# Kernel tuning notes

Hardware: AMD Instinct MI355X
Metric: run time of the kernel (lower is better)

The kernel has to match this reference:

```python
import jax, jax.numpy as jnp
import numpy as np
from jax import lax

NL = 32            # number of ocean layers
NFORCING = 720     # hourly forcing steps (30 days)
DT_FORCING = 3600.0
DT = 60.0
NSUB = 60          # dt_forcing // dt
FC_VAL = 1e-4      # Coriolis frequency [s^-1]


def setup_inputs() -> dict:
    key = jax.random.key(0)
    k1, k2, k3 = jax.random.split(key, 3)
    # pk = log(K); keep K in a physically sane range via offset
    pk = jax.random.normal(k1, (2 * NL,), dtype=jnp.float32) * 0.5 - 10.0
    TAx = jax.random.normal(k2, (NFORCING,), dtype=jnp.float32) * 0.1  # wind stress [N/m^2]
    TAy = jax.random.normal(k3, (NFORCING,), dtype=jnp.float32) * 0.1
    fc = jnp.full((1,), FC_VAL, dtype=jnp.float32)
    return {"pk": pk, "TAx": TAx, "TAy": TAy, "fc": fc}


def _vector_field(t, U, V, f, K, TAx, TAy):
    # temporal interpolation of forcing (matches original index arithmetic)
    it = jnp.asarray(t // DT, jnp.int32)
    itf = it // NSUB
    aa = (jnp.mod(it, NSUB) / NSUB).astype(U.dtype)
    nT = TAx.shape[0]
    itsup = jnp.where(itf + 1 >= nT, -1, itf + 1)
    TAxnow = (1 - aa) * TAx[itf] + aa * TAx[itsup]
    TAynow = (1 - aa) * TAy[itf] + aa * TAy[itsup]
    # N-layer stencil (nl > 1 branch of lax.cond), fully vectorized:
    #   layer 0   : +Kin[0]*TA       - Kout[0]*(x0 - x1)
    #   layer k   : -Kin[k]*(xk-xk-1) - Kout[k]*(xk - xk+1)
    #   layer nl-1: -Kin[-1]*(x - x_prev) - Kout[-1]*x   (i.e. x_next = 0)
    Kin, Kout = K[0::2], K[1::2]                       # [nl] each
    zero = jnp.zeros((1,), U.dtype)
    Unext = jnp.concatenate([U[1:], zero])
    Vnext = jnp.concatenate([V[1:], zero])
    dU_top = jnp.concatenate([Kin[:1] * TAxnow, -Kin[1:] * (U[1:] - U[:-1])])
    dV_top = jnp.concatenate([Kin[:1] * TAynow, -Kin[1:] * (V[1:] - V[:-1])])
    d_U = f * V + dU_top - Kout * (U - Unext)
    d_V = -f * U + dV_top - Kout * (V - Vnext)
    return d_U, d_V


def reference(pk, TAx, TAy, fc):
    nl = pk.shape[0] // 2
    K = jnp.exp(pk)
    f = fc[0]
    Nforcing = TAx.shape[0]
    U0 = jnp.zeros((Nforcing, nl), dtype=pk.dtype)
    V0 = jnp.zeros((Nforcing, nl), dtype=pk.dtype)

    def inner(carry, iin):
        Uold, Vold, iout = carry
        t = iout * DT_FORCING + iin * DT
        d_U, d_V = _vector_field(t, Uold, Vold, f, K, TAx, TAy)
        return (Uold + DT * d_U, Vold + DT * d_V, iout), None

    def outer(carry, iout):
        U, V = carry
        (u, v, _), _ = lax.scan(inner, (U[iout], V[iout], iout),
                                jnp.arange(NSUB))
        # last write (iout+1 == Nforcing) is out-of-bounds -> dropped,
        # exactly as in the original .at[].set semantics
        U = U.at[iout + 1].set(u)
        V = V.at[iout + 1].set(v)
        return (U, V), None

    (U, V), _ = lax.scan(outer, (U0, V0), jnp.arange(Nforcing))
    return U, V
```

## Files before the change

kernel.cpp:

```cpp
#include <hip/hip_runtime.h>
#include <hip/hip_bf16.h>

#define NLAYERS 32
#define NFORC   720
#define NSUB    60
#define DTS     60.0f
#define T_CH    16
#define N_CH    45
#define MAGIC   0x1234ABCD
#define SD      34


__device__ __forceinline__ bool sniff_bf16(const void* pk_raw, int lane) {
    const __hip_bfloat16* pk_bf = (const __hip_bfloat16*)pk_raw;
    const float v = __bfloat162float(pk_bf[lane]);
    return __all(v > -30.0f && v < -1.0f);
}

__device__ __forceinline__ void load_mrow(const float2* sMat, int i, int h, float2* R) {
    const float4* rp = (const float4*)(sMat + i * SD + h * 16);
    #pragma unroll
    for (int jj = 0; jj < 8; ++jj) {
        const float4 v = rp[jj];
        R[2 * jj]     = make_float2(v.x, v.y);
        R[2 * jj + 1] = make_float2(v.z, v.w);
    }
}

__device__ __forceinline__ float2 rmatvec(const float2* R, float2 x, int hbase) {
    float a0 = 0.f, a1 = 0.f, a2 = 0.f, a3 = 0.f;
    #pragma unroll
    for (int jj = 0; jj < 16; ++jj) {
        const float xr = __shfl(x.x, hbase + jj);
        const float xi = __shfl(x.y, hbase + jj);
        const float2 m = R[jj];
        a0 = fmaf(m.x, xr, a0);
        a1 = fmaf(m.y, xi, a1);
        a2 = fmaf(m.x, xi, a2);
        a3 = fmaf(m.y, xr, a3);
    }
    float yr = a0 - a1, yi = a2 + a3;
    yr += __shfl_xor(yr, 32);
    yi += __shfl_xor(yi, 32);
    return make_float2(yr, yi);
}

__device__ __forceinline__ void cmatmul8(float2* D, const float2* A, const float2* B, int tt) {
    if ((unsigned)tt < 128u) {
        const int i = tt >> 2, j0 = (tt & 3) * 8;
        float ar[8], ai[8];
        #pragma unroll
        for (int m = 0; m < 8; ++m) { ar[m] = 0.f; ai[m] = 0.f; }
        #pragma unroll 4
        for (int k = 0; k < 32; ++k) {
            const float2 a = A[i * SD + k];
            const float4* bp = (const float4*)(B + k * SD + j0);
            #pragma unroll
            for (int m = 0; m < 4; ++m) {
                const float4 b = bp[m];
                ar[2*m]   = fmaf(a.x, b.x, fmaf(-a.y, b.y, ar[2*m]));
                ai[2*m]   = fmaf(a.x, b.y, fmaf( a.y, b.x, ai[2*m]));
                ar[2*m+1] = fmaf(a.x, b.z, fmaf(-a.y, b.w, ar[2*m+1]));
                ai[2*m+1] = fmaf(a.x, b.w, fmaf( a.y, b.z, ai[2*m+1]));
            }
        }
        float4* dp = (float4*)(D + i * SD + j0);
        #pragma unroll
        for (int m = 0; m < 4; ++m)
            dp[m] = make_float4(ar[2*m], ai[2*m], ar[2*m+1], ai[2*m+1]);
    }
}

__global__ __launch_bounds__(1024, 1)
void junsteak_one(const void* pk_raw, const void* tax_raw, const void* tay_raw,
                  const void* fc_raw, float2* ws_z, int* ws_flag, void* out_raw)
{
    __shared__ __align__(16) float2 sM [NLAYERS * SD];
    __shared__ __align__(16) float2 sB1[NLAYERS * SD];
    __shared__ __align__(16) float2 sB2[NLAYERS * SD];
    __shared__ __align__(16) float2 sCX[NFORC];
    __shared__ __align__(16) float2 sZL[(N_CH - 1) * NLAYERS];
    __shared__ __align__(16) float4 sPQ[NLAYERS];

    const int t = threadIdx.x, lane = t & 63, wv = t >> 6;
    const int l = lane & 31, h = lane >> 5, col = 2 * wv + h;
    const int c = blockIdx.x;
    const int hbase = 16 * h;

    const bool bf = sniff_bf16(pk_raw, lane);

    float kin, kout, f, dtkin0;
    if (bf) {
        const __hip_bfloat16* pk = (const __hip_bfloat16*)pk_raw;
        kin    = expf(__bfloat162float(pk[2 * l]));
        kout   = expf(__bfloat162float(pk[2 * l + 1]));
        f      = __bfloat162float(((const __hip_bfloat16*)fc_raw)[0]);
        dtkin0 = DTS * expf(__bfloat162float(pk[0]));
        const __hip_bfloat16* tx = (const __hip_bfloat16*)tax_raw;
        const __hip_bfloat16* ty = (const __hip_bfloat16*)tay_raw;
        if (t < NFORC)
            sCX[t] = make_float2(__bfloat162float(tx[t]), __bfloat162float(ty[t]));
    } else {
        const float* pk = (const float*)pk_raw;
        kin    = expf(pk[2 * l]);
        kout   = expf(pk[2 * l + 1]);
        f      = ((const float*)fc_raw)[0];
        dtkin0 = DTS * expf(pk[0]);
        const float* tx = (const float*)tax_raw;
        const float* ty = (const float*)tay_raw;
        if (t < NFORC) sCX[t] = make_float2(tx[t], ty[t]);
    }

    __hip_bfloat16* out_bf = (__hip_bfloat16*)out_raw;
    float*          out_f  = (float*)out_raw;
    const int VOFF = NFORC * NLAYERS;

    if (c == 0 && t < 64) {
        const int off = (t >= 32 ? VOFF : 0) + (t & 31);
        if (bf) out_bf[off] = __float2bfloat16(0.0f); else out_f[off] = 0.0f;
    }

    {
        float xr = (l == col) ? 1.0f : 0.0f, xi = 0.0f;
        float Pr = 0.f, Pi = 0.f, Qr = 0.f, Qi = 0.f;
        const bool row0 = (l == 0), row31 = (l == 31);
        for (int m = 0; m < NSUB; ++m) {
            const float cp = dtkin0 * (float)(m + 1) * (1.0f / 60.0f);
            const float cq = dtkin0 * (float)(NSUB - 1 - m) * (1.0f / 60.0f);
            Pr = fmaf(cp, xr, Pr); Pi = fmaf(cp, xi, Pi);
            Qr = fmaf(cq, xr, Qr); Qi = fmaf(cq, xi, Qi);
            float xrm = __shfl_up(xr, 1);
            float xim = __shfl_up(xi, 1);
            float xrp = __shfl_down(xr, 1);
            float xip = __shfl_down(xi, 1);
            if (row31) { xrp = 0.0f; xip = 0.0f; }
            const float Lr = row0 ? (-kout * (xr - xrp))
                                  : (-kin * (xr - xrm) - kout * (xr - xrp));
            const float Li = row0 ? (-kout * (xi - xip))
                                  : (-kin * (xi - xim) - kout * (xi - xip));
            const float nxr = xr + DTS * Lr + DTS * f * xi;
            const float nxi = xi + DTS * Li - DTS * f * xr;
            xr = nxr; xi = nxi;
        }
        sM[l * SD + col] = make_float2(xr, xi);
        if (wv == 0 && h == 0) sPQ[l] = make_float4(Pr, Pi, Qr, Qi);
    }
    __syncthreads();

    float4 pq = make_float4(0.f, 0.f, 0.f, 0.f);
    float2 Mreg[16];
    float2 x = make_float2(0.0f, 0.0f);
    const int a    = c * T_CH;
    const int bend = min(a + T_CH, NFORC - 1);

    if (wv == 0) {
        pq = sPQ[l];
        load_mrow(sM, l, h, Mreg);
        float2 cn = sCX[a];
        for (int s = a; s < bend; ++s) {
            const float2 cs = cn;
            cn = sCX[s + 1];
            const float2 y = rmatvec(Mreg, x, hbase);
            const float gr = pq.x * cs.x - pq.y * cs.y + pq.z * cn.x - pq.w * cn.y;
            const float gi = pq.x * cs.y + pq.y * cs.x + pq.z * cn.y + pq.w * cn.x;
            x = make_float2(y.x + gr, y.y + gi);
        }
        if (h == 0) {
            unsigned long long zu;
            __builtin_memcpy(&zu, &x, 8);
            __hip_atomic_store((unsigned long long*)(ws_z + c * NLAYERS + l), zu,
                               __ATOMIC_RELAXED, __HIP_MEMORY_SCOPE_AGENT);
        }
        __threadfence();
        if (lane == 0)
            __hip_atomic_store(ws_flag + c, (int)MAGIC,
                               __ATOMIC_RELEASE, __HIP_MEMORY_SCOPE_AGENT);
    } else {
        cmatmul8(sB1, sM, sM, t - 64);
    }
    __syncthreads();

    if (wv == 0) {
        if (c > 0) {
            int v;
            do {
                v = (lane < c) ? __hip_atomic_load(ws_flag + lane, __ATOMIC_ACQUIRE,
                                                   __HIP_MEMORY_SCOPE_AGENT)
                               : (int)MAGIC;
            } while (!__all(v == (int)MAGIC));
            for (int idx = lane; idx < c * NLAYERS; idx += 64) {
                const unsigned long long zu =
                    __hip_atomic_load((const unsigned long long*)(ws_z + idx),
                                      __ATOMIC_RELAXED, __HIP_MEMORY_SCOPE_AGENT);
                float2 z;
                __builtin_memcpy(&z, &zu, 8);
                sZL[idx] = z;
            }
        }
    } else {
        cmatmul8(sB2, sB1, sB1, t - 64);
    }
    __syncthreads();

    if (wv != 0) cmatmul8(sB1, sB2, sB2, t - 64);
    __syncthreads();
    if (wv != 0) cmatmul8(sB2, sB1, sB1, t - 64);
    __syncthreads();

    if (t >= 64) return;

    {
        float2 Ereg[16];
        load_mrow(sB2, l, h, Ereg);
        x = make_float2(0.0f, 0.0f);
        for (int j = 0; j < c; ++j) {
            const float2 z = sZL[j * NLAYERS + l];
            const float2 y = rmatvec(Ereg, x, hbase);
            x = make_float2(y.x + z.x, y.y + z.y);
        }
    }

    {
        float2 cn = sCX[a];
        for (int s = a; s < bend; ++s) {
            const float2 cs = cn;
            cn = sCX[s + 1];
            const float2 y = rmatvec(Mreg, x, hbase);
            const float gr = pq.x * cs.x - pq.y * cs.y + pq.z * cn.x - pq.w * cn.y;
            const float gi = pq.x * cs.y + pq.y * cs.x + pq.z * cn.y + pq.w * cn.x;
            x = make_float2(y.x + gr, y.y + gi);
            if (h == 0) {
                const int row = (s + 1) * NLAYERS + l;
                if (bf) {
                    out_bf[row]        = __float2bfloat16(x.x);
                    out_bf[VOFF + row] = __float2bfloat16(x.y);
                } else {
                    out_f[row]        = x.x;
                    out_f[VOFF + row] = x.y;
                }
            }
        }
    }
}

extern "C" void kernel_launch(void* const* d_in, const int* in_sizes, int n_in,
                              void* d_out, int out_size, void* d_ws, size_t ws_size,
                              hipStream_t stream) {
    (void)in_sizes; (void)n_in; (void)out_size; (void)ws_size;
    float2* ws_z   = (float2*)d_ws;
    int*    ws_flg = (int*)((char*)d_ws + (size_t)N_CH * NLAYERS * sizeof(float2));
    junsteak_one<<<dim3(N_CH), dim3(1024), 0, stream>>>(
        d_in[0], d_in[1], d_in[2], d_in[3], ws_z, ws_flg, d_out);
}
```

Measured before the change: 112.7 us.

## Diagonalize layer operator via tridiagonal eigensolve to replace complex matrix powers

Replaces the dense 32x32 complex step-matrix construction and repeated squaring with an eigendecomposition. The symmetrized tridiagonal diffusion operator is solved by multisection bisection plus inverse iteration, so the chunk recurrence becomes scalar complex multiplies per eigenmode. Outputs are mapped back with a real 32x32 eigenvector matvec spread across waves. Chunks grow to 32 steps on 23 blocks of 512 threads, and intra-block handoff uses LDS flags in place of barriers. This assumes the Coriolis term commutes with the diffusion operator and that float32 eigenvectors are accurate enough, which risks numerical error for clustered eigenvalues.

```diff
diff --git a/kernel.cpp b/kernel.cpp
--- a/kernel.cpp
+++ b/kernel.cpp
@@ -4,170 +4,252 @@
 #define NLAYERS 32
 #define NFORC   720
 #define NSUB    60
-#define DTS     60.0f
-#define T_CH    16
-#define N_CH    45
+#define T_CH    32
+#define N_CH    23
 #define MAGIC   0x1234ABCD
-#define SD      34
-
-
+#define GSTR    36
+
+
+__device__ __forceinline__ float rl(float v, int i) {
+    return __int_as_float(__builtin_amdgcn_readlane(__float_as_int(v), i));
+}
+__device__ __forceinline__ float guardf(float x) {
+    const float ax = fabsf(x);
+    return (ax < 1e-28f) ? ((x < 0.f) ? -1e-28f : 1e-28f) : x;
+}
 __device__ __forceinline__ bool sniff_bf16(const void* pk_raw, int lane) {
     const __hip_bfloat16* pk_bf = (const __hip_bfloat16*)pk_raw;
     const float v = __bfloat162float(pk_bf[lane]);
     return __all(v > -30.0f && v < -1.0f);
 }
-
-__device__ __forceinline__ void load_mrow(const float2* sMat, int i, int h, float2* R) {
-    const float4* rp = (const float4*)(sMat + i * SD + h * 16);
-    #pragma unroll
-    for (int jj = 0; jj < 8; ++jj) {
-        const float4 v = rp[jj];
-        R[2 * jj]     = make_float2(v.x, v.y);
-        R[2 * jj + 1] = make_float2(v.z, v.w);
-    }
-}
-
-__device__ __forceinline__ float2 rmatvec(const float2* R, float2 x, int hbase) {
-    float a0 = 0.f, a1 = 0.f, a2 = 0.f, a3 = 0.f;
-    #pragma unroll
-    for (int jj = 0; jj < 16; ++jj) {
-        const float xr = __shfl(x.x, hbase + jj);
-        const float xi = __shfl(x.y, hbase + jj);
-        const float2 m = R[jj];
-        a0 = fmaf(m.x, xr, a0);
-        a1 = fmaf(m.y, xi, a1);
-        a2 = fmaf(m.x, xi, a2);
-        a3 = fmaf(m.y, xr, a3);
-    }
-    float yr = a0 - a1, yi = a2 + a3;
-    yr += __shfl_xor(yr, 32);
-    yi += __shfl_xor(yi, 32);
-    return make_float2(yr, yi);
-}
-
-__device__ __forceinline__ void cmatmul8(float2* D, const float2* A, const float2* B, int tt) {
-    if ((unsigned)tt < 128u) {
-        const int i = tt >> 2, j0 = (tt & 3) * 8;
-        float ar[8], ai[8];
-        #pragma unroll
-        for (int m = 0; m < 8; ++m) { ar[m] = 0.f; ai[m] = 0.f; }
-        #pragma unroll 4
-        for (int k = 0; k < 32; ++k) {
-            const float2 a = A[i * SD + k];
-            const float4* bp = (const float4*)(B + k * SD + j0);
-            #pragma unroll
-            for (int m = 0; m < 4; ++m) {
-                const float4 b = bp[m];
-                ar[2*m]   = fmaf(a.x, b.x, fmaf(-a.y, b.y, ar[2*m]));
-                ai[2*m]   = fmaf(a.x, b.y, fmaf( a.y, b.x, ai[2*m]));
-                ar[2*m+1] = fmaf(a.x, b.z, fmaf(-a.y, b.w, ar[2*m+1]));
-                ai[2*m+1] = fmaf(a.x, b.w, fmaf( a.y, b.z, ai[2*m+1]));
-            }
-        }
-        float4* dp = (float4*)(D + i * SD + j0);
-        #pragma unroll
-        for (int m = 0; m < 4; ++m)
-            dp[m] = make_float4(ar[2*m], ai[2*m], ar[2*m+1], ai[2*m+1]);
-    }
-}
-
-__global__ __launch_bounds__(1024, 1)
-void junsteak_one(const void* pk_raw, const void* tax_raw, const void* tay_raw,
+__device__ __forceinline__ void lds_wait_ge(int* p, int target) {
+    while (__hip_atomic_load(p, __ATOMIC_ACQUIRE, __HIP_MEMORY_SCOPE_WORKGROUP) < target)
+        __builtin_amdgcn_s_sleep(2);
+}
+
+__global__ __launch_bounds__(512, 1)
+void junsteak_eig(const void* pk_raw, const void* tax_raw, const void* tay_raw,
                   const void* fc_raw, float2* ws_z, int* ws_flag, void* out_raw)
 {
-    __shared__ __align__(16) float2 sM [NLAYERS * SD];
-    __shared__ __align__(16) float2 sB1[NLAYERS * SD];
-    __shared__ __align__(16) float2 sB2[NLAYERS * SD];
-    __shared__ __align__(16) float2 sCX[NFORC];
-    __shared__ __align__(16) float2 sZL[(N_CH - 1) * NLAYERS];
-    __shared__ __align__(16) float4 sPQ[NLAYERS];
+    __shared__ __align__(16) float  sLam[NLAYERS];
+    __shared__ __align__(16) float  sEh [NLAYERS];
+    __shared__ __align__(16) float2 sMu [NLAYERS];
+    __shared__ __align__(16) float2 sAl [NLAYERS];
+    __shared__ __align__(16) float2 sBe [NLAYERS];
+    __shared__ __align__(16) float  sG  [NLAYERS * GSTR];
+    __shared__ __align__(16) float2 sCXW[T_CH + 1];
+    __shared__ __align__(16) float2 sP1 [T_CH * NLAYERS];
+    __shared__ __align__(16) float2 sWH [T_CH * NLAYERS];
+    __shared__ __align__(16) float2 sZL [(N_CH - 1) * NLAYERS];
+    __shared__ int sZrdy, sWrdy;
 
     const int t = threadIdx.x, lane = t & 63, wv = t >> 6;
-    const int l = lane & 31, h = lane >> 5, col = 2 * wv + h;
+    const int l = lane & 31, h = lane >> 5;
     const int c = blockIdx.x;
-    const int hbase = 16 * h;
+
+    if (t == 0) { sZrdy = 0; sWrdy = 0; }
 
     const bool bf = sniff_bf16(pk_raw, lane);
 
-    float kin, kout, f, dtkin0;
+    float pkin, pkout, f;
     if (bf) {
         const __hip_bfloat16* pk = (const __hip_bfloat16*)pk_raw;
-        kin    = expf(__bfloat162float(pk[2 * l]));
-        kout   = expf(__bfloat162float(pk[2 * l + 1]));
-        f      = __bfloat162float(((const __hip_bfloat16*)fc_raw)[0]);
-        dtkin0 = DTS * expf(__bfloat162float(pk[0]));
-        const __hip_bfloat16* tx = (const __hip_bfloat16*)tax_raw;
-        const __hip_bfloat16* ty = (const __hip_bfloat16*)tay_raw;
-        if (t < NFORC)
-            sCX[t] = make_float2(__bfloat162float(tx[t]), __bfloat162float(ty[t]));
+        pkin  = __bfloat162float(pk[2 * l]);
+        pkout = __bfloat162float(pk[2 * l + 1]);
+        f     = __bfloat162float(((const __hip_bfloat16*)fc_raw)[0]);
     } else {
         const float* pk = (const float*)pk_raw;
-        kin    = expf(pk[2 * l]);
-        kout   = expf(pk[2 * l + 1]);
-        f      = ((const float*)fc_raw)[0];
-        dtkin0 = DTS * expf(pk[0]);
-        const float* tx = (const float*)tax_raw;
-        const float* ty = (const float*)tay_raw;
-        if (t < NFORC) sCX[t] = make_float2(tx[t], ty[t]);
+        pkin  = pk[2 * l];
+        pkout = pk[2 * l + 1];
+        f     = ((const float*)fc_raw)[0];
+    }
+    const float myKin  = 60.0f * expf(pkin);
+    const float myKout = 60.0f * expf(pkout);
+    const float dtf    = 60.0f * f;
+    const float dtkin0 = rl(myKin, 0);
+
+    const int a      = c * T_CH;
+    const int bend   = min(a + T_CH, NFORC - 1);
+    const int nsteps = bend - a;
+
+    if (t <= T_CH) {
+        const int idx = min(a + t, NFORC - 1);
+        if (bf) {
+            const __hip_bfloat16* tx = (const __hip_bfloat16*)tax_raw;
+            const __hip_bfloat16* ty = (const __hip_bfloat16*)tay_raw;
+            sCXW[t] = make_float2(__bfloat162float(tx[idx]), __bfloat162float(ty[idx]));
+        } else {
+            const float* tx = (const float*)tax_raw;
+            const float* ty = (const float*)tay_raw;
+            sCXW[t] = make_float2(tx[idx], ty[idx]);
+        }
     }
 
     __hip_bfloat16* out_bf = (__hip_bfloat16*)out_raw;
     float*          out_f  = (float*)out_raw;
     const int VOFF = NFORC * NLAYERS;
-
     if (c == 0 && t < 64) {
         const int off = (t >= 32 ? VOFF : 0) + (t & 31);
         if (bf) out_bf[off] = __float2bfloat16(0.0f); else out_f[off] = 0.0f;
     }
 
+    float Dd[32], Ee2[31];
     {
-        float xr = (l == col) ? 1.0f : 0.0f, xi = 0.0f;
-        float Pr = 0.f, Pi = 0.f, Qr = 0.f, Qi = 0.f;
-        const bool row0 = (l == 0), row31 = (l == 31);
-        for (int m = 0; m < NSUB; ++m) {
-            const float cp = dtkin0 * (float)(m + 1) * (1.0f / 60.0f);
-            const float cq = dtkin0 * (float)(NSUB - 1 - m) * (1.0f / 60.0f);
-            Pr = fmaf(cp, xr, Pr); Pi = fmaf(cp, xi, Pi);
-            Qr = fmaf(cq, xr, Qr); Qi = fmaf(cq, xi, Qi);
-            float xrm = __shfl_up(xr, 1);
-            float xim = __shfl_up(xi, 1);
-            float xrp = __shfl_down(xr, 1);
-            float xip = __shfl_down(xi, 1);
-            if (row31) { xrp = 0.0f; xip = 0.0f; }
-            const float Lr = row0 ? (-kout * (xr - xrp))
-                                  : (-kin * (xr - xrm) - kout * (xr - xrp));
-            const float Li = row0 ? (-kout * (xi - xip))
-                                  : (-kin * (xi - xim) - kout * (xi - xip));
-            const float nxr = xr + DTS * Lr + DTS * f * xi;
-            const float nxi = xi + DTS * Li - DTS * f * xr;
-            xr = nxr; xi = nxi;
-        }
-        sM[l * SD + col] = make_float2(xr, xi);
-        if (wv == 0 && h == 0) sPQ[l] = make_float4(Pr, Pi, Qr, Qi);
+        const float myd = (l == 0) ? -myKout : -(myKin + myKout);
+        #pragma unroll
+        for (int i = 0; i < 32; ++i) Dd[i] = rl(myd, i);
+        #pragma unroll
+        for (int i = 0; i < 31; ++i) Ee2[i] = rl(myKin, i + 1) * rl(myKout, i);
+    }
+    float lo0 = 1e30f, hi0 = -1e30f;
+    {
+        float pe = 0.f;
+        #pragma unroll
+        for (int i = 0; i < 32; ++i) {
+            const float ce = (i < 31) ? sqrtf(Ee2[i]) : 0.f;
+            lo0 = fminf(lo0, Dd[i] - (pe + ce));
+            hi0 = fmaxf(hi0, Dd[i] + (pe + ce));
+            pe = ce;
+        }
+        const float m1 = 1e-3f;
+        lo0 -= m1 * fabsf(lo0) + 1e-9f;
+        hi0 += m1 * fabsf(hi0) + 1e-9f;
+    }
+
+    {
+        const int g = lane >> 4;
+        const int k = 4 * wv + g;
+        const int j = lane & 15;
+        float lo = lo0, hi = hi0;
+        for (int r = 0; r < 7; ++r) {
+            const float x = lo + (hi - lo) * (float)(j + 1) * (1.0f / 17.0f);
+            float qq = Dd[0] - x;
+            int cnt = (qq < 0.f) ? 1 : 0;
+            #pragma unroll
+            for (int i = 1; i < 32; ++i) {
+                qq = guardf(qq);
+                qq = Dd[i] - x - __fdividef(Ee2[i - 1], qq);
+                cnt += (qq < 0.f) ? 1 : 0;
+            }
+            const unsigned long long bl = __ballot(cnt <= k);
+            const unsigned long long bh = __ballot(cnt >= k + 1);
+            const unsigned int ml = (unsigned int)((bl >> (16 * g)) & 0xFFFFu);
+            const unsigned int mh = (unsigned int)((bh >> (16 * g)) & 0xFFFFu);
+            const float w = hi - lo;
+            float nlo = lo, nhi = hi;
+            if (ml) nlo = lo + w * (float)(32 - __clz((int)ml)) * (1.0f / 17.0f);
+            if (mh) nhi = lo + w * (float)(__ffs((int)mh)) * (1.0f / 17.0f);
+            lo = nlo; hi = nhi;
+        }
+        if (j == 0) {
+            const float lam = 0.5f * (lo + hi);
+            sLam[k] = lam + (float)(k - 16) * 1e-9f * fabsf(lam);
+        }
     }
     __syncthreads();
 
-    float4 pq = make_float4(0.f, 0.f, 0.f, 0.f);
-    float2 Mreg[16];
-    float2 x = make_float2(0.0f, 0.0f);
-    const int a    = c * T_CH;
-    const int bend = min(a + T_CH, NFORC - 1);
-
     if (wv == 0) {
-        pq = sPQ[l];
-        load_mrow(sM, l, h, Mreg);
-        float2 cn = sCX[a];
-        for (int s = a; s < bend; ++s) {
-            const float2 cs = cn;
-            cn = sCX[s + 1];
-            const float2 y = rmatvec(Mreg, x, hbase);
-            const float gr = pq.x * cs.x - pq.y * cs.y + pq.z * cn.x - pq.w * cn.y;
-            const float gi = pq.x * cs.y + pq.y * cs.x + pq.z * cn.y + pq.w * cn.x;
-            x = make_float2(y.x + gr, y.y + gi);
-        }
-        if (h == 0) {
+        const float lam = sLam[l];
+        float Ee[31];
+        #pragma unroll
+        for (int i = 0; i < 31; ++i) Ee[i] = sqrtf(Ee2[i]);
+        float v[32], cp[32];
+        #pragma unroll
+        for (int i = 0; i < 32; ++i) v[i] = (i == l) ? 1.0f : 0.05f;
+        #pragma unroll
+        for (int it = 0; it < 2; ++it) {
+            float den = guardf(Dd[0] - lam);
+            cp[0] = __fdividef(Ee[0], den);
+            v[0]  = __fdividef(v[0], den);
+            #pragma unroll
+            for (int i = 1; i < 32; ++i) {
+                den = guardf(Dd[i] - lam - Ee[i - 1] * cp[i - 1]);
+                if (i < 31) cp[i] = __fdividef(Ee[i], den);
+                v[i] = __fdividef(v[i] - Ee[i - 1] * v[i - 1], den);
+            }
+            #pragma unroll
+            for (int i = 30; i >= 0; --i) v[i] = v[i] - cp[i] * v[i + 1];
+            float nrm = 0.f;
+            #pragma unroll
+            for (int i = 0; i < 32; ++i) nrm = fmaf(v[i], v[i], nrm);
+            const float inv = rsqrtf(fmaxf(nrm, 1e-30f));
+            #pragma unroll
+            for (int i = 0; i < 32; ++i) v[i] *= inv;
+        }
+        float pk2p1 = 0.f, pk2p2 = 0.f;
+        if (bf) {
+            const __hip_bfloat16* pk = (const __hip_bfloat16*)pk_raw;
+            pk2p1 = __bfloat162float(pk[2 * l + 1]);
+            if (l < 31) pk2p2 = __bfloat162float(pk[2 * l + 2]);
+        } else {
+            const float* pk = (const float*)pk_raw;
+            pk2p1 = pk[2 * l + 1];
+            if (l < 31) pk2p2 = pk[2 * l + 2];
+        }
+        const float tj = pk2p2 - pk2p1;
+        float lnD = 0.f;
+        #pragma unroll
+        for (int j = 0; j < 31; ++j) lnD += (j < l) ? rl(tj, j) : 0.f;
+        const float Dq = expf(0.5f * lnD);
+        if (lane < 32) {
+            #pragma unroll
+            for (int qq = 0; qq < 32; ++qq)
+                sG[qq * GSTR + l] = rl(Dq, qq) * v[qq];
+            sEh[l] = v[0];
+        }
+    } else if (wv == 1) {
+        const float lam = sLam[l];
+        const float ar = 1.0f + lam, ai = -dtf;
+        float pwr = 1.f, pwi = 0.f;
+        float alr = 0.f, ali = 0.f, ber = 0.f, bei = 0.f;
+        for (int m = NSUB - 1; m >= 0; --m) {
+            const float ca = 1.0f - (float)m * (1.0f / 60.0f);
+            const float cb = (float)m * (1.0f / 60.0f);
+            alr = fmaf(ca, pwr, alr); ali = fmaf(ca, pwi, ali);
+            ber = fmaf(cb, pwr, ber); bei = fmaf(cb, pwi, bei);
+            const float nr = pwr * ar - pwi * ai;
+            const float ni = pwr * ai + pwi * ar;
+            pwr = nr; pwi = ni;
+        }
+        if (lane < 32) {
+            sMu[l] = make_float2(pwr, pwi);
+            sAl[l] = make_float2(alr, ali);
+            sBe[l] = make_float2(ber, bei);
+        }
+    }
+    __syncthreads();
+
+    const int q = l;
+    float Grow[16];
+    {
+        const float4* gp = (const float4*)(sG + q * GSTR + 16 * h);
+        #pragma unroll
+        for (int j = 0; j < 4; ++j) {
+            const float4 g4 = gp[j];
+            Grow[4 * j + 0] = g4.x; Grow[4 * j + 1] = g4.y;
+            Grow[4 * j + 2] = g4.z; Grow[4 * j + 3] = g4.w;
+        }
+    }
+
+    if (wv == 0) {
+        const float2 mu = sMu[l];
+        const float  s0 = dtkin0 * sEh[l];
+        const float2 al = sAl[l], be = sBe[l];
+        const float2 ph = make_float2(s0 * al.x, s0 * al.y);
+        const float2 qh = make_float2(s0 * be.x, s0 * be.y);
+        float2 w = make_float2(0.f, 0.f);
+        for (int m = 0; m < nsteps; ++m) {
+            const float2 cs = sCXW[m], cn = sCXW[m + 1];
+            const float gr = ph.x * cs.x - ph.y * cs.y + qh.x * cn.x - qh.y * cn.y;
+            const float gi = ph.x * cs.y + ph.y * cs.x + qh.x * cn.y + qh.y * cn.x;
+            const float wr = w.x * mu.x - w.y * mu.y + gr;
+            const float wi = w.x * mu.y + w.y * mu.x + gi;
+            w = make_float2(wr, wi);
+            if (lane < 32) sP1[m * NLAYERS + l] = w;
+        }
+        if (lane < 32) {
             unsigned long long zu;
-            __builtin_memcpy(&zu, &x, 8);
+            __builtin_memcpy(&zu, &w, 8);
             __hip_atomic_store((unsigned long long*)(ws_z + c * NLAYERS + l), zu,
                                __ATOMIC_RELAXED, __HIP_MEMORY_SCOPE_AGENT);
         }
@@ -175,19 +257,45 @@
         if (lane == 0)
             __hip_atomic_store(ws_flag + c, (int)MAGIC,
                                __ATOMIC_RELEASE, __HIP_MEMORY_SCOPE_AGENT);
-    } else {
-        cmatmul8(sB1, sM, sM, t - 64);
-    }
-    __syncthreads();
-
-    if (wv == 0) {
+
+        float2 muT = mu;
+        #pragma unroll
+        for (int r = 0; r < 5; ++r) {
+            const float nr = muT.x * muT.x - muT.y * muT.y;
+            const float ni = 2.0f * muT.x * muT.y;
+            muT = make_float2(nr, ni);
+        }
+
+        lds_wait_ge(&sZrdy, 1);
+        float2 b = make_float2(0.f, 0.f);
+        for (int j = 0; j < c; ++j) {
+            const float2 z = sZL[j * NLAYERS + l];
+            const float br = b.x * muT.x - b.y * muT.y + z.x;
+            const float bi = b.x * muT.y + b.y * muT.x + z.y;
+            b = make_float2(br, bi);
+        }
+        float2 cur = b;
+        for (int m = 0; m < nsteps; ++m) {
+            const float nr = cur.x * mu.x - cur.y * mu.y;
+            const float ni = cur.x * mu.y + cur.y * mu.x;
+            cur = make_float2(nr, ni);
+            if (lane < 32) {
+                const float2 p1 = sP1[m * NLAYERS + l];
+                sWH[m * NLAYERS + l] = make_float2(p1.x + cur.x, p1.y + cur.y);
+            }
+        }
+        if (lane == 0)
+            __hip_atomic_store(&sWrdy, 1, __ATOMIC_RELEASE, __HIP_MEMORY_SCOPE_WORKGROUP);
+    } else if (wv == 1) {
         if (c > 0) {
             int v;
             do {
                 v = (lane < c) ? __hip_atomic_load(ws_flag + lane, __ATOMIC_ACQUIRE,
                                                    __HIP_MEMORY_SCOPE_AGENT)
                                : (int)MAGIC;
-            } while (!__all(v == (int)MAGIC));
+                if (__all(v == (int)MAGIC)) break;
+                __builtin_amdgcn_s_sleep(2);
+            } while (true);
             for (int idx = lane; idx < c * NLAYERS; idx += 64) {
                 const unsigned long long zu =
                     __hip_atomic_load((const unsigned long long*)(ws_z + idx),
@@ -197,46 +305,39 @@
                 sZL[idx] = z;
             }
         }
-    } else {
-        cmatmul8(sB2, sB1, sB1, t - 64);
-    }
-    __syncthreads();
-
-    if (wv != 0) cmatmul8(sB1, sB2, sB2, t - 64);
-    __syncthreads();
-    if (wv != 0) cmatmul8(sB2, sB1, sB1, t - 64);
-    __syncthreads();
-
-    if (t >= 64) return;
-
-    {
-        float2 Ereg[16];
-        load_mrow(sB2, l, h, Ereg);
-        x = make_float2(0.0f, 0.0f);
-        for (int j = 0; j < c; ++j) {
-            const float2 z = sZL[j * NLAYERS + l];
-            const float2 y = rmatvec(Ereg, x, hbase);
-            x = make_float2(y.x + z.x, y.y + z.y);
-        }
-    }
-
-    {
-        float2 cn = sCX[a];
-        for (int s = a; s < bend; ++s) {
-            const float2 cs = cn;
-            cn = sCX[s + 1];
-            const float2 y = rmatvec(Mreg, x, hbase);
-            const float gr = pq.x * cs.x - pq.y * cs.y + pq.z * cn.x - pq.w * cn.y;
-            const float gi = pq.x * cs.y + pq.y * cs.x + pq.z * cn.y + pq.w * cn.x;
-            x = make_float2(y.x + gr, y.y + gi);
-            if (h == 0) {
-                const int row = (s + 1) * NLAYERS + l;
+        if (lane == 0)
+            __hip_atomic_store(&sZrdy, 1, __ATOMIC_RELEASE, __HIP_MEMORY_SCOPE_WORKGROUP);
+    }
+
+    lds_wait_ge(&sWrdy, 1);
+    #pragma unroll
+    for (int r = 0; r < 4; ++r) {
+        const int m = 4 * wv + r;
+        if (m < nsteps) {
+            float2 wh[16];
+            const float4* wp = (const float4*)(sWH + m * NLAYERS + 16 * h);
+            #pragma unroll
+            for (int j = 0; j < 8; ++j) {
+                const float4 t4 = wp[j];
+                wh[2 * j]     = make_float2(t4.x, t4.y);
+                wh[2 * j + 1] = make_float2(t4.z, t4.w);
+            }
+            float yr = 0.f, yi = 0.f;
+            #pragma unroll
+            for (int j = 0; j < 16; ++j) {
+                yr = fmaf(Grow[j], wh[j].x, yr);
+                yi = fmaf(Grow[j], wh[j].y, yi);
+            }
+            yr += __shfl_xor(yr, 32);
+            yi += __shfl_xor(yi, 32);
+            if (lane < 32) {
+                const int row = (a + m + 1) * NLAYERS + q;
                 if (bf) {
-                    out_bf[row]        = __float2bfloat16(x.x);
-                    out_bf[VOFF + row] = __float2bfloat16(x.y);
+                    out_bf[row]        = __float2bfloat16(yr);
+                    out_bf[VOFF + row] = __float2bfloat16(yi);
                 } else {
-                    out_f[row]        = x.x;
-                    out_f[VOFF + row] = x.y;
+                    out_f[row]        = yr;
+                    out_f[VOFF + row] = yi;
                 }
             }
         }
@@ -249,6 +350,6 @@
     (void)in_sizes; (void)n_in; (void)out_size; (void)ws_size;
     float2* ws_z   = (float2*)d_ws;
     int*    ws_flg = (int*)((char*)d_ws + (size_t)N_CH * NLAYERS * sizeof(float2));
-    junsteak_one<<<dim3(N_CH), dim3(1024), 0, stream>>>(
+    junsteak_eig<<<dim3(N_CH), dim3(512), 0, stream>>>(
         d_in[0], d_in[1], d_in[2], d_in[3], ws_z, ws_flg, d_out);
 }
```

Result: faster. 94.24 us (-16.4%).
